# Kernel tuning notes

Hardware: AMD Instinct MI355X
Metric: run time of the kernel (lower is better)

## Reference

```python
import jax, jax.numpy as jnp
import numpy as np
import math

D_MODEL = 1024
N_HEADS = 16
D_K = D_MODEL // N_HEADS
HIDDEN = 4096
R_SOFTPLUS_0 = 1.442695041
EPS = 1e-6


def setup_inputs() -> dict:
    key = jax.random.key(0)
    ks = jax.random.split(key, 16)
    B, S = 4, 2048
    s = 0.02
    inp = {
        "inputs": jax.random.normal(ks[0], (B, S, D_MODEL), jnp.float32),
        "mask": jnp.zeros((1, 1, S, S), jnp.float32),
        # RmsNorm (direct_scale=True -> init 1.0)
        "rms_scale": jnp.ones((D_MODEL,), jnp.float32),
        # attention projections (torch Linear: y = x @ W.T + b)
        "Wq": jax.random.normal(ks[1], (D_MODEL, D_MODEL), jnp.float32) * s,
        "bq": jnp.zeros((D_MODEL,), jnp.float32),
        "Wk": jax.random.normal(ks[2], (D_MODEL, D_MODEL), jnp.float32) * s,
        "bk": jnp.zeros((D_MODEL,), jnp.float32),
        "Wv": jax.random.normal(ks[3], (D_MODEL, D_MODEL), jnp.float32) * s,
        "bv": jnp.zeros((D_MODEL,), jnp.float32),
        "per_dim_scale": jnp.zeros((D_K,), jnp.float32),
        "Wpost": jax.random.normal(ks[4], (D_MODEL, D_MODEL), jnp.float32) * s,
        "bpost": jnp.zeros((D_MODEL,), jnp.float32),
        # FFN LayerNorm (direct_scale=False -> scale param init 0, effective 1+scale)
        "ln_scale": jnp.zeros((D_MODEL,), jnp.float32),
        "ln_bias": jnp.zeros((D_MODEL,), jnp.float32),
        "W1": jax.random.normal(ks[5], (HIDDEN, D_MODEL), jnp.float32) * s,
        "b1": jnp.zeros((HIDDEN,), jnp.float32),
        "W2": jax.random.normal(ks[6], (D_MODEL, HIDDEN), jnp.float32) * s,
        "b2": jnp.zeros((D_MODEL,), jnp.float32),
    }
    return inp


def _rms_norm(x, scale):
    ms = jnp.mean(x * x, axis=-1, keepdims=True)
    return x * jax.lax.rsqrt(ms + EPS) * scale


def _layer_norm(x, scale, bias):
    mean = jnp.mean(x, axis=-1, keepdims=True)
    var = jnp.mean((x - mean) ** 2, axis=-1, keepdims=True)
    return (x - mean) * jax.lax.rsqrt(var + EPS) * (1.0 + scale) + bias


def reference(inputs, mask, rms_scale, Wq, bq, Wk, bk, Wv, bv, per_dim_scale,
              Wpost, bpost, ln_scale, ln_bias, W1, b1, W2, b2):
    B, S, _ = inputs.shape
    x = _rms_norm(inputs, rms_scale)
    # projections -> [B, H, S, Dk]
    def split_heads(t):
        return t.reshape(B, S, N_HEADS, D_K).transpose(0, 2, 1, 3)
    q = split_heads(x @ Wq.T + bq)
    k = split_heads(x @ Wk.T + bk)
    v = split_heads(x @ Wv.T + bv)
    # PerDimScale: (r_softplus_0 / sqrt(d_k)) * softplus(param)
    scale = (R_SOFTPLUS_0 / math.sqrt(D_K)) * jax.nn.softplus(per_dim_scale)
    q = q * scale
    attn = jnp.einsum("bhqd,bhkd->bhqk", q, k) + mask
    attn = jax.nn.softmax(attn, axis=-1)
    out = jnp.einsum("bhqk,bhkd->bhqd", attn, v)
    out = out.transpose(0, 2, 1, 3).reshape(B, S, D_MODEL)
    attn_out = out @ Wpost.T + bpost
    h = attn_out + inputs  # residual (dropout=0)
    # FeedForward with pre-LayerNorm and residual
    y = _layer_norm(h, ln_scale, ln_bias)
    y = jax.nn.relu(y @ W1.T + b1)
    y = y @ W2.T + b2
    return y + h
```

## Files before the change

### kernel.cpp

```cpp
#include <hip/hip_runtime.h>
#include <hip/hip_bf16.h>

typedef unsigned short u16;
typedef __attribute__((ext_vector_type(8))) short short8;
typedef __attribute__((ext_vector_type(4))) float floatx4;

#define R_PDS 0.18033688f
#define LOG2E 1.4426950408889634f

__device__ __forceinline__ float bf2f(u16 u) {
    union { float f; unsigned int i; } c; c.i = ((unsigned int)u) << 16; return c.f;
}
__device__ __forceinline__ u16 f2b(float f) {
    union { float f; unsigned int i; } c; c.f = f;
    unsigned int r = c.i + 0x7fffu + ((c.i >> 16) & 1u);
    return (u16)(r >> 16);
}
__device__ __forceinline__ unsigned int pk2(float a, float b) {
    __hip_bfloat162 h = __float22bfloat162_rn(float2{a, b});
    unsigned int u; __builtin_memcpy(&u, &h, 4); return u;
}

__device__ __forceinline__ void async16(const u16* g, u16* l) {
    __builtin_amdgcn_global_load_lds(
        (const __attribute__((address_space(1))) unsigned int*)g,
        (__attribute__((address_space(3))) unsigned int*)l, 16, 0, 0);
}

__global__ __launch_bounds__(256) void f2b_all_k(const float* __restrict__ Wq, const float* __restrict__ Wk,
                                                 const float* __restrict__ Wv, const float* __restrict__ Wp,
                                                 const float* __restrict__ W1, const float* __restrict__ W2,
                                                 u16* __restrict__ Wqkvb, u16* __restrict__ Wpb,
                                                 u16* __restrict__ W1b,  u16* __restrict__ W2b,
                                                 int* flag) {
    int bid = blockIdx.x;
    if (bid == 0 && threadIdx.x == 0) *flag = 0;
    const float* src; u16* dst; int off;
    if      (bid < 1024) { src = Wq; dst = Wqkvb;                off = bid; }
    else if (bid < 2048) { src = Wk; dst = Wqkvb + 1024 * 1024;  off = bid - 1024; }
    else if (bid < 3072) { src = Wv; dst = Wqkvb + 2048 * 1024;  off = bid - 2048; }
    else if (bid < 4096) { src = Wp; dst = Wpb;                  off = bid - 3072; }
    else if (bid < 8192) { src = W1; dst = W1b;                  off = bid - 4096; }
    else                 { src = W2; dst = W2b;                  off = bid - 8192; }
    int i = off * 256 + threadIdx.x;
    float4 v = ((const float4*)src)[i];
    uint2 w; w.x = pk2(v.x, v.y); w.y = pk2(v.z, v.w);
    ((uint2*)dst)[i] = w;
}

__global__ __launch_bounds__(256) void mask_any_k(const float* __restrict__ mask, int* flag) {
    int i = blockIdx.x * 256 + threadIdx.x;
    uint4 u = ((const uint4*)mask)[i];
    unsigned int v = (u.x | u.y | u.z | u.w) & 0x7fffffffu;
    if (v) atomicOr(flag, 1);
}

__global__ __launch_bounds__(256) void rmsnorm_k(const float* __restrict__ in,
                                                 const float* __restrict__ gscale,
                                                 u16* __restrict__ out) {
    int row = blockIdx.x;
    int t = threadIdx.x, lane = t & 63, wave = t >> 6;
    const float* x = in + (size_t)row * 1024;
    float4 v = *(const float4*)(x + t * 4);
    float ss = v.x*v.x + v.y*v.y + v.z*v.z + v.w*v.w;
    for (int o = 1; o < 64; o <<= 1) ss += __shfl_xor(ss, o, 64);
    __shared__ float red[4];
    if (lane == 0) red[wave] = ss;
    __syncthreads();
    float tot = red[0] + red[1] + red[2] + red[3];
    float inv = rsqrtf(tot * (1.0f / 1024.0f) + 1e-6f);
    float4 s = *(const float4*)(gscale + t * 4);
    uint2 w;
    w.x = pk2(v.x * inv * s.x, v.y * inv * s.y);
    w.y = pk2(v.z * inv * s.z, v.w * inv * s.w);
    *(uint2*)(out + (size_t)row * 1024 + t * 4) = w;
}

__global__ __launch_bounds__(256) void layernorm_k(const u16* __restrict__ in,
                                                   const float* __restrict__ gs,
                                                   const float* __restrict__ gb,
                                                   u16* __restrict__ out) {
    int row = blockIdx.x;
    int t = threadIdx.x, lane = t & 63, wave = t >> 6;
    const u16* x = in + (size_t)row * 1024;
    uint2 u = *(const uint2*)(x + t * 4);
    float v0 = bf2f((u16)(u.x & 0xffff)), v1 = bf2f((u16)(u.x >> 16));
    float v2 = bf2f((u16)(u.y & 0xffff)), v3 = bf2f((u16)(u.y >> 16));
    float s1 = v0 + v1 + v2 + v3;
    float s2 = v0*v0 + v1*v1 + v2*v2 + v3*v3;
    for (int o = 1; o < 64; o <<= 1) { s1 += __shfl_xor(s1, o, 64); s2 += __shfl_xor(s2, o, 64); }
    __shared__ float r1[4], r2[4];
    if (lane == 0) { r1[wave] = s1; r2[wave] = s2; }
    __syncthreads();
    float mean = (r1[0] + r1[1] + r1[2] + r1[3]) * (1.0f / 1024.0f);
    float var  = (r2[0] + r2[1] + r2[2] + r2[3]) * (1.0f / 1024.0f) - mean * mean;
    var = fmaxf(var, 0.0f);
    float inv = rsqrtf(var + 1e-6f);
    float4 sc = *(const float4*)(gs + t * 4);
    float4 bb = *(const float4*)(gb + t * 4);
    uint2 w;
    w.x = pk2((v0 - mean) * inv * (1.0f + sc.x) + bb.x,
              (v1 - mean) * inv * (1.0f + sc.y) + bb.y);
    w.y = pk2((v2 - mean) * inv * (1.0f + sc.z) + bb.z,
              (v3 - mean) * inv * (1.0f + sc.w) + bb.w);
    *(uint2*)(out + (size_t)row * 1024 + t * 4) = w;
}

template <int EPI, bool OUTF32, bool RESF32>
__global__ __launch_bounds__(256) void gemm_bt_k(const u16* __restrict__ A,
                                                 const u16* __restrict__ B,
                                                 const float* __restrict__ bias,
                                                 const void* __restrict__ res,
                                                 void* __restrict__ Cv,
                                                 int M, int N, int K) {
    __shared__ __align__(16) u16 As[4096];
    __shared__ __align__(16) u16 Bs[4096];
    const int t = threadIdx.x, wave = t >> 6, lane = t & 63;
    const int quad = lane >> 4, ln = lane & 15;
    const int m0 = blockIdx.y * 128, n0 = blockIdx.x * 128;
    const int wm = (wave >> 1) * 64, wn = (wave & 1) * 64;

    floatx4 acc[4][4];
    for (int mt = 0; mt < 4; mt++) for (int nt = 0; nt < 4; nt++) acc[mt][nt] = (floatx4)0.0f;

    const int c0 = t, c1 = t + 256;
    const u16* Ap0 = A + (size_t)(m0 + (c0 >> 2)) * K + (c0 & 3) * 8;
    const u16* Ap1 = A + (size_t)(m0 + (c1 >> 2)) * K + (c1 & 3) * 8;
    const u16* Bp0 = B + (size_t)(n0 + (c0 >> 2)) * K + (c0 & 3) * 8;
    const u16* Bp1 = B + (size_t)(n0 + (c1 >> 2)) * K + (c1 & 3) * 8;
    u16* AsW0 = As + wave * 512;
    u16* AsW1 = As + 2048 + wave * 512;
    u16* BsW0 = Bs + wave * 512;
    u16* BsW1 = Bs + 2048 + wave * 512;

    for (int kt = 0; kt < K; kt += 32) {
        __syncthreads();
        async16(Ap0 + kt, AsW0);
        async16(Ap1 + kt, AsW1);
        async16(Bp0 + kt, BsW0);
        async16(Bp1 + kt, BsW1);
        __syncthreads();
        short8 af[4], bfr[4];
        for (int mt = 0; mt < 4; mt++)
            af[mt] = *(const short8*)&As[(wm + mt * 16 + ln) * 32 + quad * 8];
        for (int nt = 0; nt < 4; nt++)
            bfr[nt] = *(const short8*)&Bs[(wn + nt * 16 + ln) * 32 + quad * 8];
        for (int mt = 0; mt < 4; mt++)
            for (int nt = 0; nt < 4; nt++)
                acc[mt][nt] = __builtin_amdgcn_mfma_f32_16x16x32_bf16(af[mt], bfr[nt], acc[mt][nt], 0, 0, 0);
    }

    for (int nt = 0; nt < 4; nt++) {
        int col = n0 + wn + nt * 16 + ln;
        float bv = bias[col];
        for (int mt = 0; mt < 4; mt++) {
            for (int r = 0; r < 4; r++) {
                int row = m0 + wm + mt * 16 + quad * 4 + r;
                float v = acc[mt][nt][r] + bv;
                if (EPI == 1) v = fmaxf(v, 0.0f);
                if (EPI == 2) {
                    if (RESF32) v += ((const float*)res)[(size_t)row * N + col];
                    else        v += bf2f(((const u16*)res)[(size_t)row * N + col]);
                }
                if (OUTF32) ((float*)Cv)[(size_t)row * N + col] = v;
                else        ((u16*)Cv)[(size_t)row * N + col] = f2b(v);
            }
        }
    }
}

__global__ __launch_bounds__(256) void gemm_qkv_k(const u16* __restrict__ A,
                                                  const u16* __restrict__ B,
                                                  const float* __restrict__ bq,
                                                  const float* __restrict__ bk,
                                                  const float* __restrict__ bv,
                                                  const float* __restrict__ pds,
                                                  u16* __restrict__ C) {
    const int K = 1024, N = 3072;
    __shared__ __align__(16) u16 As[4096];
    __shared__ __align__(16) u16 Bs[4096];
    const int t = threadIdx.x, wave = t >> 6, lane = t & 63;
    const int quad = lane >> 4, ln = lane & 15;
    const int m0 = blockIdx.y * 128, n0 = blockIdx.x * 128;
    const int wm = (wave >> 1) * 64, wn = (wave & 1) * 64;

    floatx4 acc[4][4];
    for (int mt = 0; mt < 4; mt++) for (int nt = 0; nt < 4; nt++) acc[mt][nt] = (floatx4)0.0f;

    const int c0 = t, c1 = t + 256;
    const u16* Ap0 = A + (size_t)(m0 + (c0 >> 2)) * K + (c0 & 3) * 8;
    const u16* Ap1 = A + (size_t)(m0 + (c1 >> 2)) * K + (c1 & 3) * 8;
    const u16* Bp0 = B + (size_t)(n0 + (c0 >> 2)) * K + (c0 & 3) * 8;
    const u16* Bp1 = B + (size_t)(n0 + (c1 >> 2)) * K + (c1 & 3) * 8;
    u16* AsW0 = As + wave * 512;
    u16* AsW1 = As + 2048 + wave * 512;
    u16* BsW0 = Bs + wave * 512;
    u16* BsW1 = Bs + 2048 + wave * 512;

    for (int kt = 0; kt < K; kt += 32) {
        __syncthreads();
        async16(Ap0 + kt, AsW0);
        async16(Ap1 + kt, AsW1);
        async16(Bp0 + kt, BsW0);
        async16(Bp1 + kt, BsW1);
        __syncthreads();
        short8 af[4], bfr[4];
        for (int mt = 0; mt < 4; mt++)
            af[mt] = *(const short8*)&As[(wm + mt * 16 + ln) * 32 + quad * 8];
        for (int nt = 0; nt < 4; nt++)
            bfr[nt] = *(const short8*)&Bs[(wn + nt * 16 + ln) * 32 + quad * 8];
        for (int mt = 0; mt < 4; mt++)
            for (int nt = 0; nt < 4; nt++)
                acc[mt][nt] = __builtin_amdgcn_mfma_f32_16x16x32_bf16(af[mt], bfr[nt], acc[mt][nt], 0, 0, 0);
    }

    for (int nt = 0; nt < 4; nt++) {
        int col = n0 + wn + nt * 16 + ln;
        float bv_, sc = 1.0f;
        if (col < 1024) {
            bv_ = bq[col];
            float xp = pds[col & 63];
            float sp = (xp > 20.0f) ? xp : log1pf(__expf(xp));
            sc = R_PDS * sp * LOG2E;
        } else if (col < 2048) bv_ = bk[col - 1024];
        else                   bv_ = bv[col - 2048];
        for (int mt = 0; mt < 4; mt++)
            for (int r = 0; r < 4; r++) {
                int row = m0 + wm + mt * 16 + quad * 4 + r;
                C[(size_t)row * N + col] = f2b((acc[mt][nt][r] + bv_) * sc);
            }
    }
}

__global__ __launch_bounds__(256) void transpose_v_k(const u16* __restrict__ qkv, u16* __restrict__ vT) {
    __shared__ u16 tile[64][65];
    int st = blockIdx.x, bh = blockIdx.y;
    int b = bh >> 4, h = bh & 15;
    const u16* vb = qkv + (size_t)(b * 2048 + st * 64) * 3072 + 2048 + h * 64;
    int t = threadIdx.x;
    for (int i = t; i < 4096; i += 256) {
        int s = i >> 6, d = i & 63;
        tile[s][d] = vb[(size_t)s * 3072 + d];
    }
    __syncthreads();
    u16* ob = vT + (size_t)bh * 131072 + st * 64;
    for (int i = t; i < 4096; i += 256) {
        int d = i >> 6, s = i & 63;
        ob[(size_t)d * 2048 + s] = tile[s][d];
    }
}

__global__ __launch_bounds__(256) void attn_k(const u16* __restrict__ qkv,
                                              const u16* __restrict__ vT,
                                              const float* __restrict__ mask,
                                              const int* __restrict__ flag,
                                              u16* __restrict__ o) {
    __shared__ __align__(16) u16 QPs[128][72];
    __shared__ __align__(16) u16 Ks[64][72];
    __shared__ __align__(16) u16 Vs[64][72];

    const int t = threadIdx.x, wave = t >> 6, lane = t & 63;
    const int quad = lane >> 4, ln = lane & 15;
    const int qt = blockIdx.x, bh = blockIdx.y;
    const int b = bh >> 4, h = bh & 15;
    const int q0 = qt * 128;
    const int wm = wave * 32;

    const u16* qb = qkv + (size_t)(b * 2048 + q0) * 3072 + h * 64;
    for (int c = t; c < 1024; c += 256) {
        int row = c >> 3, seg = c & 7;
        *(uint4*)&QPs[row][seg * 8] = *(const uint4*)(qb + (size_t)row * 3072 + seg * 8);
    }
    __syncthreads();

    short8 qf[2][2];
    for (int mt = 0; mt < 2; mt++)
        for (int ks = 0; ks < 2; ks++)
            qf[mt][ks] = *(const short8*)&QPs[wm + mt * 16 + ln][ks * 32 + quad * 8];

    short8 ones_f;
    for (int i = 0; i < 8; i++) ones_f[i] = (short)0x3F80;

    floatx4 acc_o[2][4], acc_l[2];
    for (int mt = 0; mt < 2; mt++) {
        acc_l[mt] = (floatx4)0.0f;
        for (int dt = 0; dt < 4; dt++) acc_o[mt][dt] = (floatx4)0.0f;
    }

    const int mflag = *flag;
    const u16* kb = qkv + (size_t)(b * 2048) * 3072 + 1024 + h * 64;
    const u16* vg = vT + (size_t)bh * 131072;

    const int r0 = t >> 3, s0 = (t & 7) * 8;
    const u16* kp0 = kb + (size_t)r0 * 3072 + s0;
    const u16* kp1 = kb + (size_t)(r0 + 32) * 3072 + s0;
    const u16* vp0 = vg + (size_t)r0 * 2048 + s0;
    const u16* vp1 = vg + (size_t)(r0 + 32) * 2048 + s0;

    uint4 kr0 = *(const uint4*)(kp0);
    uint4 kr1 = *(const uint4*)(kp1);
    uint4 vr0 = *(const uint4*)(vp0);
    uint4 vr1 = *(const uint4*)(vp1);

    for (int kv0 = 0; kv0 < 2048; kv0 += 64) {
        __syncthreads();
        *(uint4*)&Ks[r0][s0]      = kr0;
        *(uint4*)&Ks[r0 + 32][s0] = kr1;
        *(uint4*)&Vs[r0][s0]      = vr0;
        *(uint4*)&Vs[r0 + 32][s0] = vr1;
        __syncthreads();
        if (kv0 + 64 < 2048) {
            size_t ko = (size_t)(kv0 + 64) * 3072;
            int    vo = kv0 + 64;
            kr0 = *(const uint4*)(kp0 + ko);
            kr1 = *(const uint4*)(kp1 + ko);
            vr0 = *(const uint4*)(vp0 + vo);
            vr1 = *(const uint4*)(vp1 + vo);
        }

        for (int nt = 0; nt < 4; nt++) {
            floatx4 sa0 = (floatx4)0.0f, sa1 = (floatx4)0.0f;
            for (int ks = 0; ks < 2; ks++) {
                short8 kf = *(const short8*)&Ks[nt * 16 + ln][ks * 32 + quad * 8];
                sa0 = __builtin_amdgcn_mfma_f32_16x16x32_bf16(kf, qf[0][ks], sa0, 0, 0, 0);
                sa1 = __builtin_amdgcn_mfma_f32_16x16x32_bf16(kf, qf[1][ks], sa1, 0, 0, 0);
            }
            if (mflag) {
                for (int r = 0; r < 4; r++) {
                    int kc = kv0 + nt * 16 + quad * 4 + r;
                    sa0[r] += mask[(size_t)(q0 + wm + ln) * 2048 + kc] * LOG2E;
                    sa1[r] += mask[(size_t)(q0 + wm + 16 + ln) * 2048 + kc] * LOG2E;
                }
            }
            {
                uint2 w;
                w.x = pk2(__builtin_amdgcn_exp2f(fminf(sa0[0], 80.0f)),
                          __builtin_amdgcn_exp2f(fminf(sa0[1], 80.0f)));
                w.y = pk2(__builtin_amdgcn_exp2f(fminf(sa0[2], 80.0f)),
                          __builtin_amdgcn_exp2f(fminf(sa0[3], 80.0f)));
                *(uint2*)&QPs[wm + ln][nt * 16 + quad * 4] = w;
            }
            {
                uint2 w;
                w.x = pk2(__builtin_amdgcn_exp2f(fminf(sa1[0], 80.0f)),
                          __builtin_amdgcn_exp2f(fminf(sa1[1], 80.0f)));
                w.y = pk2(__builtin_amdgcn_exp2f(fminf(sa1[2], 80.0f)),
                          __builtin_amdgcn_exp2f(fminf(sa1[3], 80.0f)));
                *(uint2*)&QPs[wm + 16 + ln][nt * 16 + quad * 4] = w;
            }
        }

        for (int ks = 0; ks < 2; ks++) {
            short8 a0 = *(const short8*)&QPs[wm + ln][ks * 32 + quad * 8];
            short8 a1 = *(const short8*)&QPs[wm + 16 + ln][ks * 32 + quad * 8];
            acc_l[0] = __builtin_amdgcn_mfma_f32_16x16x32_bf16(a0, ones_f, acc_l[0], 0, 0, 0);
            acc_l[1] = __builtin_amdgcn_mfma_f32_16x16x32_bf16(a1, ones_f, acc_l[1], 0, 0, 0);
            for (int dt = 0; dt < 4; dt++) {
                short8 bfr = *(const short8*)&Vs[dt * 16 + ln][ks * 32 + quad * 8];
                acc_o[0][dt] = __builtin_amdgcn_mfma_f32_16x16x32_bf16(a0, bfr, acc_o[0][dt], 0, 0, 0);
                acc_o[1][dt] = __builtin_amdgcn_mfma_f32_16x16x32_bf16(a1, bfr, acc_o[1][dt], 0, 0, 0);
            }
        }
    }

    u16* ob = o + (size_t)(b * 2048 + q0) * 1024 + h * 64;
    for (int mt = 0; mt < 2; mt++) {
        for (int r = 0; r < 4; r++) {
            float inv = 1.0f / acc_l[mt][r];
            int row = wm + mt * 16 + quad * 4 + r;
            for (int dt = 0; dt < 4; dt++)
                ob[(size_t)row * 1024 + dt * 16 + ln] = f2b(acc_o[mt][dt][r] * inv);
        }
    }
}

extern "C" void kernel_launch(void* const* d_in, const int* in_sizes, int n_in,
                              void* d_out, int out_size, void* d_ws, size_t ws_size,
                              hipStream_t stream) {
    const float* inp    = (const float*)d_in[0];
    const float* mask   = (const float*)d_in[1];
    const float* rms_s  = (const float*)d_in[2];
    const float* Wq     = (const float*)d_in[3];
    const float* bq     = (const float*)d_in[4];
    const float* Wk     = (const float*)d_in[5];
    const float* bk     = (const float*)d_in[6];
    const float* Wv     = (const float*)d_in[7];
    const float* bv     = (const float*)d_in[8];
    const float* pds    = (const float*)d_in[9];
    const float* Wpost  = (const float*)d_in[10];
    const float* bpost  = (const float*)d_in[11];
    const float* ln_s   = (const float*)d_in[12];
    const float* ln_b   = (const float*)d_in[13];
    const float* W1     = (const float*)d_in[14];
    const float* b1     = (const float*)d_in[15];
    const float* W2     = (const float*)d_in[16];
    const float* b2     = (const float*)d_in[17];
    float* out = (float*)d_out;

    char* w = (char*)d_ws;
    const size_t MB = 1u << 20;
    u16* W1b   = (u16*)(w + 0 * MB);
    u16* W2b   = (u16*)(w + 8 * MB);
    u16* qkv   = (u16*)(w + 16 * MB);
    u16* x     = (u16*)(w + 64 * MB);
    u16* o     = (u16*)(w + 64 * MB);
    u16* Wqkvb = (u16*)(w + 80 * MB);
    u16* Wpb   = (u16*)(w + 86 * MB);
    u16* yln   = (u16*)(w + 80 * MB);
    u16* vT    = (u16*)(w + 96 * MB);
    u16* hb    = (u16*)(w + 96 * MB);
    u16* f1    = (u16*)(w + 16 * MB);
    int* flag  = (int*)(w + 112 * MB);

    f2b_all_k<<<12288, 256, 0, stream>>>(Wq, Wk, Wv, Wpost, W1, W2, Wqkvb, Wpb, W1b, W2b, flag);
    mask_any_k<<<4096, 256, 0, stream>>>(mask, flag);

    rmsnorm_k<<<8192, 256, 0, stream>>>(inp, rms_s, x);

    gemm_qkv_k<<<dim3(24, 64), 256, 0, stream>>>(x, Wqkvb, bq, bk, bv, pds, qkv);

    transpose_v_k<<<dim3(32, 64), 256, 0, stream>>>(qkv, vT);

    attn_k<<<dim3(16, 64), 256, 0, stream>>>(qkv, vT, mask, flag, o);

    gemm_bt_k<2, false, true><<<dim3(8, 64), 256, 0, stream>>>(o, Wpb, bpost, inp, hb, 8192, 1024, 1024);

    layernorm_k<<<8192, 256, 0, stream>>>(hb, ln_s, ln_b, yln);

    gemm_bt_k<1, false, true><<<dim3(32, 64), 256, 0, stream>>>(yln, W1b, b1, nullptr, f1, 8192, 4096, 1024);
    gemm_bt_k<2, true, false><<<dim3(8, 64), 256, 0, stream>>>(f1, W2b, b2, hb, out, 8192, 1024, 4096);
}
```

Measured before the change: 594.7 us.

## Replace GEMMs with 256x256 double-buffered 8-wave pipelined MFMA kernel

All GEMMs (QKV, output projection, FFN up and down) move from a 128x128 tile with 4 waves and a single LDS buffer to a 256x256 tile with 8 waves. The new kernel uses a K-step of 64, double-buffered LDS filled by async global-to-LDS loads, an XOR-swizzled LDS layout to avoid bank conflicts, and interleaved prefetch with barriers and setprio. An XCD-aware block swizzle improves L2 locality. The aim is to raise MFMA utilization and cut per-iteration sync and global traffic. In exchange it uses 128KB of LDS per block and many accumulator registers, and the smaller grids risk tail imbalance.

```diff
diff --git a/kernel.cpp b/kernel.cpp
--- a/kernel.cpp
+++ b/kernel.cpp
@@ -106,116 +106,170 @@
     *(uint2*)(out + (size_t)row * 1024 + t * 4) = w;
 }
 
-template <int EPI, bool OUTF32, bool RESF32>
-__global__ __launch_bounds__(256) void gemm_bt_k(const u16* __restrict__ A,
-                                                 const u16* __restrict__ B,
-                                                 const float* __restrict__ bias,
-                                                 const void* __restrict__ res,
-                                                 void* __restrict__ Cv,
-                                                 int M, int N, int K) {
-    __shared__ __align__(16) u16 As[4096];
-    __shared__ __align__(16) u16 Bs[4096];
+__device__ __forceinline__ void gemm8_core(const u16* __restrict__ A, const u16* __restrict__ B,
+                                           int K, int NG, int m0, int n0,
+                                           u16* lds, floatx4 (&acc)[8][4]) {
     const int t = threadIdx.x, wave = t >> 6, lane = t & 63;
     const int quad = lane >> 4, ln = lane & 15;
-    const int m0 = blockIdx.y * 128, n0 = blockIdx.x * 128;
-    const int wm = (wave >> 1) * 64, wn = (wave & 1) * 64;
-
-    floatx4 acc[4][4];
-    for (int mt = 0; mt < 4; mt++) for (int nt = 0; nt < 4; nt++) acc[mt][nt] = (floatx4)0.0f;
-
-    const int c0 = t, c1 = t + 256;
-    const u16* Ap0 = A + (size_t)(m0 + (c0 >> 2)) * K + (c0 & 3) * 8;
-    const u16* Ap1 = A + (size_t)(m0 + (c1 >> 2)) * K + (c1 & 3) * 8;
-    const u16* Bp0 = B + (size_t)(n0 + (c0 >> 2)) * K + (c0 & 3) * 8;
-    const u16* Bp1 = B + (size_t)(n0 + (c1 >> 2)) * K + (c1 & 3) * 8;
-    u16* AsW0 = As + wave * 512;
-    u16* AsW1 = As + 2048 + wave * 512;
-    u16* BsW0 = Bs + wave * 512;
-    u16* BsW1 = Bs + 2048 + wave * 512;
-
-    for (int kt = 0; kt < K; kt += 32) {
-        __syncthreads();
-        async16(Ap0 + kt, AsW0);
-        async16(Ap1 + kt, AsW1);
-        async16(Bp0 + kt, BsW0);
-        async16(Bp1 + kt, BsW1);
-        __syncthreads();
-        short8 af[4], bfr[4];
-        for (int mt = 0; mt < 4; mt++)
-            af[mt] = *(const short8*)&As[(wm + mt * 16 + ln) * 32 + quad * 8];
-        for (int nt = 0; nt < 4; nt++)
-            bfr[nt] = *(const short8*)&Bs[(wn + nt * 16 + ln) * 32 + quad * 8];
-        for (int mt = 0; mt < 4; mt++)
-            for (int nt = 0; nt < 4; nt++)
-                acc[mt][nt] = __builtin_amdgcn_mfma_f32_16x16x32_bf16(af[mt], bfr[nt], acc[mt][nt], 0, 0, 0);
-    }
-
-    for (int nt = 0; nt < 4; nt++) {
-        int col = n0 + wn + nt * 16 + ln;
+    const int wave_m = wave >> 2, wave_n = wave & 3;
+
+    const int rowS = t >> 3;
+    const int srcb = ((t & 7) * 16) ^ (((t >> 3) & 7) << 4);
+    const u16* Ab = A + (size_t)(m0 + rowS) * K + (srcb >> 1);
+    const u16* Bb = B + (size_t)(n0 + rowS) * K + (srcb >> 1);
+    const size_t rstep = (size_t)64 * K;
+    const size_t hstep = (size_t)128 * K;
+    const int ldw = wave * 512;
+
+    #define STAGE_A8(buf, h, kt) do { \
+        u16* _l = lds + (buf) * 32768 + (h) * 8192 + ldw; \
+        const u16* _g = Ab + (size_t)(h) * hstep + (kt); \
+        async16(_g, _l); async16(_g + rstep, _l + 4096); } while (0)
+    #define STAGE_B8(buf, h, kt) do { \
+        u16* _l = lds + (buf) * 32768 + 16384 + (h) * 8192 + ldw; \
+        const u16* _g = Bb + (size_t)(h) * hstep + (kt); \
+        async16(_g, _l); async16(_g + rstep, _l + 4096); } while (0)
+
+    #define RD8(base, lr, ks) \
+        (*(const short8*)((base) + (lr) * 64 + ((((ks) * 64 + quad * 16) ^ (((lr) & 7) << 4)) >> 1)))
+
+    STAGE_B8(0, 0, 0); STAGE_B8(0, 1, 0);
+    STAGE_A8(0, 0, 0); STAGE_A8(0, 1, 0);
+    if (NG > 1) {
+        STAGE_B8(1, 0, 64); STAGE_B8(1, 1, 64);
+        asm volatile("s_waitcnt vmcnt(4)" ::: "memory");
+    } else {
+        asm volatile("s_waitcnt vmcnt(0)" ::: "memory");
+    }
+    __builtin_amdgcn_s_barrier();
+
+    for (int g = 0; g < NG; ++g) {
+        const int cur = g & 1;
+        const u16* aH = lds + cur * 32768 + wave_m * 8192;
+        const u16* bH = lds + cur * 32768 + 16384 + (wave_n >> 1) * 8192;
+        const int lrB = (wave_n & 1) * 64;
+        short8 bf[4][2];
+        #pragma unroll
+        for (int q = 0; q < 4; ++q) {
+            short8 af[2][2];
+            #pragma unroll
+            for (int mt = 0; mt < 2; ++mt)
+                #pragma unroll
+                for (int ks = 0; ks < 2; ++ks)
+                    af[mt][ks] = RD8(aH, q * 32 + mt * 16 + ln, ks);
+            if (q == 0) {
+                #pragma unroll
+                for (int nt = 0; nt < 4; ++nt)
+                    #pragma unroll
+                    for (int ks = 0; ks < 2; ++ks)
+                        bf[nt][ks] = RD8(bH, lrB + nt * 16 + ln, ks);
+            }
+            if (q == 0 && g + 1 < NG) STAGE_A8(cur ^ 1, 0, (g + 1) * 64);
+            if (q == 1 && g + 1 < NG) STAGE_A8(cur ^ 1, 1, (g + 1) * 64);
+            if (q == 2 && g + 2 < NG) STAGE_B8(cur, 0, (g + 2) * 64);
+            if (q == 3 && g + 2 < NG) STAGE_B8(cur, 1, (g + 2) * 64);
+            __builtin_amdgcn_s_barrier();
+            asm volatile("s_waitcnt lgkmcnt(0)" ::: "memory");
+            __builtin_amdgcn_s_setprio(1);
+            #pragma unroll
+            for (int ks = 0; ks < 2; ++ks)
+                #pragma unroll
+                for (int mt = 0; mt < 2; ++mt)
+                    #pragma unroll
+                    for (int nt = 0; nt < 4; ++nt)
+                        acc[q * 2 + mt][nt] = __builtin_amdgcn_mfma_f32_16x16x32_bf16(
+                            af[mt][ks], bf[nt][ks], acc[q * 2 + mt][nt], 0, 0, 0);
+            __builtin_amdgcn_s_setprio(0);
+            __builtin_amdgcn_sched_barrier(0);
+            if (q == 3 && g + 1 < NG) {
+                if (g + 2 < NG) asm volatile("s_waitcnt vmcnt(4)" ::: "memory");
+                else            asm volatile("s_waitcnt vmcnt(0)" ::: "memory");
+            }
+            __builtin_amdgcn_s_barrier();
+        }
+    }
+    #undef STAGE_A8
+    #undef STAGE_B8
+    #undef RD8
+}
+
+__device__ __forceinline__ void xcd_swizzle(int& bx, int& by) {
+    int gx = gridDim.x, nwg = gx * gridDim.y;
+    int lin = blockIdx.y * gx + blockIdx.x;
+    int swz = (lin & 7) * (nwg >> 3) + (lin >> 3);
+    bx = swz % gx; by = swz / gx;
+}
+
+template <int EPI, bool OUTF32, bool RESF32>
+__global__ __launch_bounds__(512, 2) void gemm8_bt_k(const u16* __restrict__ A,
+                                                     const u16* __restrict__ B,
+                                                     const float* __restrict__ bias,
+                                                     const void* __restrict__ res,
+                                                     void* __restrict__ Cv,
+                                                     int M, int N, int K) {
+    __shared__ __align__(16) u16 lds[65536];
+    int bx, by; xcd_swizzle(bx, by);
+    const int m0 = by * 256, n0 = bx * 256;
+    const int t = threadIdx.x, wave = t >> 6, lane = t & 63;
+    const int quad = lane >> 4, ln = lane & 15;
+    const int wm = (wave >> 2) * 128, wn = (wave & 3) * 64;
+
+    floatx4 acc[8][4];
+    #pragma unroll
+    for (int mf = 0; mf < 8; mf++)
+        #pragma unroll
+        for (int nf = 0; nf < 4; nf++) acc[mf][nf] = (floatx4)0.0f;
+
+    gemm8_core(A, B, K, K >> 6, m0, n0, lds, acc);
+
+    #pragma unroll
+    for (int nf = 0; nf < 4; nf++) {
+        int col = n0 + wn + nf * 16 + ln;
         float bv = bias[col];
-        for (int mt = 0; mt < 4; mt++) {
+        #pragma unroll
+        for (int mf = 0; mf < 8; mf++) {
+            int row = m0 + wm + mf * 16 + quad * 4;
+            #pragma unroll
             for (int r = 0; r < 4; r++) {
-                int row = m0 + wm + mt * 16 + quad * 4 + r;
-                float v = acc[mt][nt][r] + bv;
+                float v = acc[mf][nf][r] + bv;
                 if (EPI == 1) v = fmaxf(v, 0.0f);
                 if (EPI == 2) {
-                    if (RESF32) v += ((const float*)res)[(size_t)row * N + col];
-                    else        v += bf2f(((const u16*)res)[(size_t)row * N + col]);
+                    if (RESF32) v += ((const float*)res)[(size_t)(row + r) * N + col];
+                    else        v += bf2f(((const u16*)res)[(size_t)(row + r) * N + col]);
                 }
-                if (OUTF32) ((float*)Cv)[(size_t)row * N + col] = v;
-                else        ((u16*)Cv)[(size_t)row * N + col] = f2b(v);
-            }
-        }
-    }
-}
-
-__global__ __launch_bounds__(256) void gemm_qkv_k(const u16* __restrict__ A,
-                                                  const u16* __restrict__ B,
-                                                  const float* __restrict__ bq,
-                                                  const float* __restrict__ bk,
-                                                  const float* __restrict__ bv,
-                                                  const float* __restrict__ pds,
-                                                  u16* __restrict__ C) {
+                if (OUTF32) ((float*)Cv)[(size_t)(row + r) * N + col] = v;
+                else        ((u16*)Cv)[(size_t)(row + r) * N + col] = f2b(v);
+            }
+        }
+    }
+}
+
+__global__ __launch_bounds__(512, 2) void gemm8_qkv_k(const u16* __restrict__ A,
+                                                      const u16* __restrict__ B,
+                                                      const float* __restrict__ bq,
+                                                      const float* __restrict__ bk,
+                                                      const float* __restrict__ bv,
+                                                      const float* __restrict__ pds,
+                                                      u16* __restrict__ C) {
     const int K = 1024, N = 3072;
-    __shared__ __align__(16) u16 As[4096];
-    __shared__ __align__(16) u16 Bs[4096];
+    __shared__ __align__(16) u16 lds[65536];
+    int bx, by; xcd_swizzle(bx, by);
+    const int m0 = by * 256, n0 = bx * 256;
     const int t = threadIdx.x, wave = t >> 6, lane = t & 63;
     const int quad = lane >> 4, ln = lane & 15;
-    const int m0 = blockIdx.y * 128, n0 = blockIdx.x * 128;
-    const int wm = (wave >> 1) * 64, wn = (wave & 1) * 64;
-
-    floatx4 acc[4][4];
-    for (int mt = 0; mt < 4; mt++) for (int nt = 0; nt < 4; nt++) acc[mt][nt] = (floatx4)0.0f;
-
-    const int c0 = t, c1 = t + 256;
-    const u16* Ap0 = A + (size_t)(m0 + (c0 >> 2)) * K + (c0 & 3) * 8;
-    const u16* Ap1 = A + (size_t)(m0 + (c1 >> 2)) * K + (c1 & 3) * 8;
-    const u16* Bp0 = B + (size_t)(n0 + (c0 >> 2)) * K + (c0 & 3) * 8;
-    const u16* Bp1 = B + (size_t)(n0 + (c1 >> 2)) * K + (c1 & 3) * 8;
-    u16* AsW0 = As + wave * 512;
-    u16* AsW1 = As + 2048 + wave * 512;
-    u16* BsW0 = Bs + wave * 512;
-    u16* BsW1 = Bs + 2048 + wave * 512;
-
-    for (int kt = 0; kt < K; kt += 32) {
-        __syncthreads();
-        async16(Ap0 + kt, AsW0);
-        async16(Ap1 + kt, AsW1);
-        async16(Bp0 + kt, BsW0);
-        async16(Bp1 + kt, BsW1);
-        __syncthreads();
-        short8 af[4], bfr[4];
-        for (int mt = 0; mt < 4; mt++)
-            af[mt] = *(const short8*)&As[(wm + mt * 16 + ln) * 32 + quad * 8];
-        for (int nt = 0; nt < 4; nt++)
-            bfr[nt] = *(const short8*)&Bs[(wn + nt * 16 + ln) * 32 + quad * 8];
-        for (int mt = 0; mt < 4; mt++)
-            for (int nt = 0; nt < 4; nt++)
-                acc[mt][nt] = __builtin_amdgcn_mfma_f32_16x16x32_bf16(af[mt], bfr[nt], acc[mt][nt], 0, 0, 0);
-    }
-
-    for (int nt = 0; nt < 4; nt++) {
-        int col = n0 + wn + nt * 16 + ln;
+    const int wm = (wave >> 2) * 128, wn = (wave & 3) * 64;
+
+    floatx4 acc[8][4];
+    #pragma unroll
+    for (int mf = 0; mf < 8; mf++)
+        #pragma unroll
+        for (int nf = 0; nf < 4; nf++) acc[mf][nf] = (floatx4)0.0f;
+
+    gemm8_core(A, B, K, K >> 6, m0, n0, lds, acc);
+
+    #pragma unroll
+    for (int nf = 0; nf < 4; nf++) {
+        int col = n0 + wn + nf * 16 + ln;
         float bv_, sc = 1.0f;
         if (col < 1024) {
             bv_ = bq[col];
@@ -224,11 +278,13 @@
             sc = R_PDS * sp * LOG2E;
         } else if (col < 2048) bv_ = bk[col - 1024];
         else                   bv_ = bv[col - 2048];
-        for (int mt = 0; mt < 4; mt++)
-            for (int r = 0; r < 4; r++) {
-                int row = m0 + wm + mt * 16 + quad * 4 + r;
-                C[(size_t)row * N + col] = f2b((acc[mt][nt][r] + bv_) * sc);
-            }
+        #pragma unroll
+        for (int mf = 0; mf < 8; mf++) {
+            int row = m0 + wm + mf * 16 + quad * 4;
+            #pragma unroll
+            for (int r = 0; r < 4; r++)
+                C[(size_t)(row + r) * N + col] = f2b((acc[mf][nf][r] + bv_) * sc);
+        }
     }
 }
 
@@ -417,16 +473,16 @@
 
     rmsnorm_k<<<8192, 256, 0, stream>>>(inp, rms_s, x);
 
-    gemm_qkv_k<<<dim3(24, 64), 256, 0, stream>>>(x, Wqkvb, bq, bk, bv, pds, qkv);
+    gemm8_qkv_k<<<dim3(12, 32), 512, 0, stream>>>(x, Wqkvb, bq, bk, bv, pds, qkv);
 
     transpose_v_k<<<dim3(32, 64), 256, 0, stream>>>(qkv, vT);
 
     attn_k<<<dim3(16, 64), 256, 0, stream>>>(qkv, vT, mask, flag, o);
 
-    gemm_bt_k<2, false, true><<<dim3(8, 64), 256, 0, stream>>>(o, Wpb, bpost, inp, hb, 8192, 1024, 1024);
+    gemm8_bt_k<2, false, true><<<dim3(4, 32), 512, 0, stream>>>(o, Wpb, bpost, inp, hb, 8192, 1024, 1024);
 
     layernorm_k<<<8192, 256, 0, stream>>>(hb, ln_s, ln_b, yln);
 
-    gemm_bt_k<1, false, true><<<dim3(32, 64), 256, 0, stream>>>(yln, W1b, b1, nullptr, f1, 8192, 4096, 1024);
-    gemm_bt_k<2, true, false><<<dim3(8, 64), 256, 0, stream>>>(f1, W2b, b2, hb, out, 8192, 1024, 4096);
-}
+    gemm8_bt_k<1, false, true><<<dim3(16, 32), 512, 0, stream>>>(yln, W1b, b1, nullptr, f1, 8192, 4096, 1024);
+    gemm8_bt_k<2, true, false><<<dim3(4, 32), 512, 0, stream>>>(f1, W2b, b2, hb, out, 8192, 1024, 4096);
+}
```

After: 600.6 us. No clear change (+1.0%).
